# Kernel tuning notes

Hardware: AMD Instinct MI355X
Metric: run time of the kernel (lower is better)

Reference implementation:

```python
import jax, jax.numpy as jnp
from jax import lax
import numpy as np

B, C, L, K = 8, 512, 2048, 3
CQ = C // 8


def setup_inputs() -> dict:
    key = jax.random.key(0)
    k1, k2, k3, k4 = jax.random.split(key, 4)
    scale = 0.05
    return {
        "x": jax.random.normal(k1, (B, C, L), dtype=jnp.float32),
        "Wq": jax.random.normal(k2, (CQ, C, K), dtype=jnp.float32) * scale,
        "Wk": jax.random.normal(k3, (CQ, C, K), dtype=jnp.float32) * scale,
        "Wv": jax.random.normal(k4, (C, C, K), dtype=jnp.float32) * scale,
        "gamma": jnp.ones((1,), dtype=jnp.float32),
    }


def _conv1d(x, w):
    # x: [B, Cin, L], w: [Cout, Cin, K]; 'same' padding = (K-1)//2 on both sides
    pad = (w.shape[-1] - 1) // 2
    return lax.conv_general_dilated(
        x, w, window_strides=(1,), padding=[(pad, pad)],
        dimension_numbers=("NCH", "OIH", "NCH"))


def reference(x, Wq, Wk, Wv, gamma):
    q = _conv1d(x, Wq)  # [B, C/8, L]
    k = _conv1d(x, Wk)  # [B, C/8, L]
    v = _conv1d(x, Wv)  # [B, C, L]
    # scores[b, i, j] = sum_c q[b, c, i] * k[b, c, j]  (q^T k)
    scores = jnp.einsum("bci,bcj->bij", q, k)
    # softmax over dim=1 (the query/i axis) — non-standard axis
    beta = jax.nn.softmax(scores, axis=1)  # [B, L, L]
    out = gamma * jnp.einsum("bcl,blj->bcj", v, beta)  # [B, C, L]
    return out
```

## Files before the change

kernel.cpp:

```cpp
#include <hip/hip_runtime.h>
#include <cstddef>
#include <math.h>

#define L_DIM 2048
#define C_DIM 512
#define CQ_DIM 64
#define B_DIM 8

typedef _Float16 f16x8 __attribute__((ext_vector_type(8)));
typedef __fp16 fp16x2_t __attribute__((ext_vector_type(2)));
typedef float f32x4 __attribute__((ext_vector_type(4)));

__device__ __forceinline__ unsigned short f2h(float f) {
    union { _Float16 h; unsigned short u; } v;
    v.h = (_Float16)f;
    return v.u;
}

__device__ __forceinline__ unsigned p2u(float a, float b) {
    union { fp16x2_t h; unsigned u; } v;
    v.h = __builtin_amdgcn_cvt_pkrtz(a, b);
    return v.u;
}

__global__ __launch_bounds__(256) void prep_w(const float* __restrict__ Wq,
                                              const float* __restrict__ Wk,
                                              const float* __restrict__ Wv,
                                              unsigned short* __restrict__ Wh) {
    const int idx = blockIdx.x * 256 + threadIdx.x;
    const int ci = idx & 511;
    const int co = (idx >> 9) % 640;
    const int t  = idx / (640 * 512);
    float w;
    if (co < 64)       w = Wq[(size_t)co * 1536 + ci * 3 + t];
    else if (co < 128) w = Wk[(size_t)(co - 64) * 1536 + ci * 3 + t];
    else               w = Wv[(size_t)(co - 128) * 1536 + ci * 3 + t];
    Wh[idx] = f2h(w);
}

__global__ __launch_bounds__(256) void prep_x(const float* __restrict__ x,
                                              unsigned short* __restrict__ xT) {
    const int l0  = blockIdx.x * 64;
    const int ci0 = blockIdx.y * 64;
    const int b   = blockIdx.z;

    __shared__ float xs[64][68];
    const int tid = threadIdx.x;
    const float* xb = x + ((size_t)b * C_DIM + ci0) * L_DIM;

    for (int idx = tid; idx < 64 * 16; idx += 256) {
        int ci = idx >> 4, lq = idx & 15;
        *(float4*)&xs[ci][lq * 4] = *(const float4*)&xb[(size_t)ci * L_DIM + l0 + lq * 4];
    }
    __syncthreads();

    unsigned short* ob = xT + ((size_t)b * L_DIM + l0) * C_DIM + ci0;
    for (int idx = tid; idx < 64 * 8; idx += 256) {
        int l = idx >> 3, c8 = idx & 7;
        ushort4 r0, r1;
        r0.x = f2h(xs[c8 * 8 + 0][l]); r0.y = f2h(xs[c8 * 8 + 1][l]);
        r0.z = f2h(xs[c8 * 8 + 2][l]); r0.w = f2h(xs[c8 * 8 + 3][l]);
        r1.x = f2h(xs[c8 * 8 + 4][l]); r1.y = f2h(xs[c8 * 8 + 5][l]);
        r1.z = f2h(xs[c8 * 8 + 6][l]); r1.w = f2h(xs[c8 * 8 + 7][l]);
        *(ushort4*)&ob[(size_t)l * C_DIM + c8 * 8] = r0;
        *(ushort4*)&ob[(size_t)l * C_DIM + c8 * 8 + 4] = r1;
    }
}

__global__ __launch_bounds__(256) void conv_all(const unsigned short* __restrict__ Wh,
                                                const unsigned short* __restrict__ xT,
                                                unsigned short* __restrict__ qT,
                                                unsigned short* __restrict__ kT,
                                                unsigned short* __restrict__ vB) {
    const int l0  = blockIdx.x * 128;
    const int co0 = blockIdx.y * 64;
    const int b   = blockIdx.z;

    __shared__ unsigned short As[3][64][40];
    __shared__ unsigned short Bs[130][40];

    const int tid  = threadIdx.x;
    const int lane = tid & 63, w = tid >> 6;
    const int ln15 = lane & 15, quad = lane >> 4;

    const int co_w = (w & 1) * 32;
    const int l_w  = (w >> 1) * 64;

    const unsigned short* xb = xT + (size_t)b * L_DIM * C_DIM;

    f32x4 acc[2][4] = {};

    for (int ci0 = 0; ci0 < C_DIM; ci0 += 32) {
        __syncthreads();
        for (int idx = tid; idx < 768; idx += 256) {
            int t = idx >> 8, co = (idx >> 2) & 63, c8 = idx & 3;
            *(float4*)&As[t][co][c8 * 8] =
                *(const float4*)&Wh[(((size_t)t * 640) + co0 + co) * C_DIM + ci0 + c8 * 8];
        }
        for (int idx = tid; idx < 520; idx += 256) {
            int la = idx >> 2, c8 = idx & 3;
            int l = l0 - 1 + la;
            float4 vx = {0.f, 0.f, 0.f, 0.f};
            if (l >= 0 && l < L_DIM)
                vx = *(const float4*)&xb[(size_t)l * C_DIM + ci0 + c8 * 8];
            *(float4*)&Bs[la][c8 * 8] = vx;
        }
        __syncthreads();

#pragma unroll
        for (int t = 0; t < 3; t++) {
            f16x8 a[2], bfr[4];
#pragma unroll
            for (int ct = 0; ct < 2; ct++)
                a[ct] = *(const f16x8*)&As[t][co_w + ct * 16 + ln15][quad * 8];
#pragma unroll
            for (int lt = 0; lt < 4; lt++)
                bfr[lt] = *(const f16x8*)&Bs[l_w + lt * 16 + ln15 + t][quad * 8];
#pragma unroll
            for (int ct = 0; ct < 2; ct++)
#pragma unroll
                for (int lt = 0; lt < 4; lt++)
                    acc[ct][lt] = __builtin_amdgcn_mfma_f32_16x16x32_f16(a[ct], bfr[lt], acc[ct][lt], 0, 0, 0);
        }
    }

    if (co0 < 128) {
        unsigned short* dst = (co0 == 0 ? qT : kT) + (size_t)b * L_DIM * CQ_DIM;
#pragma unroll
        for (int ct = 0; ct < 2; ct++)
#pragma unroll
            for (int lt = 0; lt < 4; lt++) {
                const int l = l0 + l_w + lt * 16 + ln15;
                ushort4 r;
                r.x = f2h(acc[ct][lt][0]); r.y = f2h(acc[ct][lt][1]);
                r.z = f2h(acc[ct][lt][2]); r.w = f2h(acc[ct][lt][3]);
                *(ushort4*)&dst[(size_t)l * CQ_DIM + co_w + ct * 16 + quad * 4] = r;
            }
    } else {
        unsigned short* dst = vB + ((size_t)b * C_DIM + (co0 - 128)) * L_DIM;
#pragma unroll
        for (int ct = 0; ct < 2; ct++)
#pragma unroll
            for (int lt = 0; lt < 4; lt++) {
                const int l = l0 + l_w + lt * 16 + ln15;
#pragma unroll
                for (int r = 0; r < 4; r++) {
                    const int co = co_w + ct * 16 + quad * 4 + r;
                    dst[(size_t)co * L_DIM + l] = f2h(acc[ct][lt][r]);
                }
            }
    }
}

__global__ __launch_bounds__(256) void stat_k(const unsigned short* __restrict__ qT,
                                              const unsigned short* __restrict__ kT,
                                              float* __restrict__ pstat) {
    const int ich = blockIdx.x;
    const int j0  = blockIdx.y * 64;
    const int b   = blockIdx.z;

    __shared__ unsigned short sbuf[64 * 68];

    const int tid = threadIdx.x;
    const int lane = tid & 63, w = tid >> 6;
    const int ln15 = lane & 15, quad = lane >> 4;
    const int sj = w * 16;

    const unsigned short* qb = qT + (size_t)b * L_DIM * CQ_DIM;
    const unsigned short* kb = kT + (size_t)b * L_DIM * CQ_DIM;

    for (int idx = tid; idx < 64 * 8; idx += 256) {
        int r = idx >> 3, c8 = idx & 7;
        *(float4*)&sbuf[r * 68 + c8 * 8] = *(const float4*)&kb[(size_t)(j0 + r) * CQ_DIM + c8 * 8];
    }
    __syncthreads();
    f16x8 kfr[2];
#pragma unroll
    for (int cc = 0; cc < 2; cc++)
        kfr[cc] = *(const f16x8*)&sbuf[(sj + ln15) * 68 + cc * 32 + quad * 8];

    float m_run = -1e30f, l_run = 0.f;

    for (int t = 0; t < 4; t++) {
        const int i0 = ich * 256 + t * 64;
        __syncthreads();
        for (int idx = tid; idx < 64 * 8; idx += 256) {
            int r = idx >> 3, c8 = idx & 7;
            *(float4*)&sbuf[r * 68 + c8 * 8] = *(const float4*)&qb[(size_t)(i0 + r) * CQ_DIM + c8 * 8];
        }
        __syncthreads();

        f32x4 sacc[4] = {};
#pragma unroll
        for (int cc = 0; cc < 2; cc++) {
#pragma unroll
            for (int it = 0; it < 4; it++) {
                const f16x8 afr = *(const f16x8*)&sbuf[(it * 16 + ln15) * 68 + cc * 32 + quad * 8];
                sacc[it] = __builtin_amdgcn_mfma_f32_16x16x32_f16(afr, kfr[cc], sacc[it], 0, 0, 0);
            }
        }

        float bm = -1e30f;
#pragma unroll
        for (int it = 0; it < 4; it++)
#pragma unroll
            for (int r = 0; r < 4; r++)
                bm = fmaxf(bm, sacc[it][r]);
        bm = fmaxf(bm, __shfl_xor(bm, 16, 64));
        bm = fmaxf(bm, __shfl_xor(bm, 32, 64));
        const float m_new = fmaxf(m_run, bm);
        const float alpha = __expf(m_run - m_new);

        float lsum = 0.f;
#pragma unroll
        for (int it = 0; it < 4; it++) {
            float p0 = __expf(sacc[it][0] - m_new);
            float p1 = __expf(sacc[it][1] - m_new);
            float p2 = __expf(sacc[it][2] - m_new);
            float p3 = __expf(sacc[it][3] - m_new);
            lsum += (p0 + p1) + (p2 + p3);
        }
        lsum += __shfl_xor(lsum, 16, 64);
        lsum += __shfl_xor(lsum, 32, 64);
        l_run = l_run * alpha + lsum;
        m_run = m_new;
    }

    if (quad == 0) {
        const int j = j0 + sj + ln15;
        float* pm = pstat;
        float* pl = pstat + 8 * 8 * 2048;
        pm[((size_t)ich * 8 + b) * 2048 + j] = m_run;
        pl[((size_t)ich * 8 + b) * 2048 + j] = l_run;
    }
}

__global__ __launch_bounds__(256) void pv2(const unsigned short* __restrict__ qT,
                                           const unsigned short* __restrict__ kT,
                                           const unsigned short* __restrict__ vB,
                                           const float* __restrict__ pstat,
                                           const float* __restrict__ gamma,
                                           float* __restrict__ out) {
    const int j0  = blockIdx.x * 64;
    const int co0 = blockIdx.y * 128;
    const int b   = blockIdx.z;

    __shared__ unsigned short pps[64 * 68];
    __shared__ unsigned short qTs[64 * 68];
    __shared__ unsigned short vvs[128 * 68];
    __shared__ float mj_s[64];
    __shared__ float il_s[64];

    const int tid = threadIdx.x;
    const int lane = tid & 63, w = tid >> 6;
    const int ln15 = lane & 15, quad = lane >> 4;

    const unsigned short* qb = qT + (size_t)b * L_DIM * CQ_DIM;
    const unsigned short* kb = kT + (size_t)b * L_DIM * CQ_DIM;
    const unsigned short* vb = vB + (size_t)b * C_DIM * L_DIM;

    const int sj  = w * 16;
    const int wco = w * 32;

    if (tid < 64) {
        const int j = j0 + tid;
        const float* pm = pstat;
        const float* pl = pstat + 8 * 8 * 2048;
        float m = -1e30f;
        float pmv[8];
#pragma unroll
        for (int c = 0; c < 8; c++) {
            pmv[c] = pm[((size_t)c * 8 + b) * 2048 + j];
            m = fmaxf(m, pmv[c]);
        }
        float l = 0.f;
#pragma unroll
        for (int c = 0; c < 8; c++)
            l = fmaf(pl[((size_t)c * 8 + b) * 2048 + j], __expf(pmv[c] - m), l);
        mj_s[tid] = m;
        il_s[tid] = gamma[0] / l;
    }

    for (int idx = tid; idx < 64 * 8; idx += 256) {
        int r = idx >> 3, c8 = idx & 7;
        *(float4*)&pps[r * 68 + c8 * 8] = *(const float4*)&kb[(size_t)(j0 + r) * CQ_DIM + c8 * 8];
    }
    __syncthreads();
    f16x8 kfr[2];
#pragma unroll
    for (int cc = 0; cc < 2; cc++)
        kfr[cc] = *(const f16x8*)&pps[(sj + ln15) * 68 + cc * 32 + quad * 8];
    const float m_lane = mj_s[sj + ln15];
    float inv[4];
#pragma unroll
    for (int bb = 0; bb < 4; bb++)
        inv[bb] = il_s[bb * 16 + ln15];

    f32x4 oacc[2][4] = {};

    for (int i0 = 0; i0 < L_DIM; i0 += 64) {
        __syncthreads();
        for (int idx = tid; idx < 64 * 8; idx += 256) {
            int r = idx >> 3, c8 = idx & 7;
            *(float4*)&qTs[r * 68 + c8 * 8] = *(const float4*)&qb[(size_t)(i0 + r) * CQ_DIM + c8 * 8];
        }
        for (int idx = tid; idx < 128 * 8; idx += 256) {
            int r = idx >> 3, c8 = idx & 7;
            *(float4*)&vvs[r * 68 + c8 * 8] = *(const float4*)&vb[(size_t)(co0 + r) * L_DIM + i0 + c8 * 8];
        }
        __syncthreads();

        f32x4 sacc[4] = {};
        __builtin_amdgcn_s_setprio(1);
#pragma unroll
        for (int cc = 0; cc < 2; cc++) {
#pragma unroll
            for (int it = 0; it < 4; it++) {
                const f16x8 afr = *(const f16x8*)&qTs[(it * 16 + ln15) * 68 + cc * 32 + quad * 8];
                sacc[it] = __builtin_amdgcn_mfma_f32_16x16x32_f16(afr, kfr[cc], sacc[it], 0, 0, 0);
            }
        }
        __builtin_amdgcn_s_setprio(0);

        const int j = sj + ln15;
#pragma unroll
        for (int it = 0; it < 4; it++) {
            float p0 = __expf(sacc[it][0] - m_lane);
            float p1 = __expf(sacc[it][1] - m_lane);
            float p2 = __expf(sacc[it][2] - m_lane);
            float p3 = __expf(sacc[it][3] - m_lane);
            uint2 u;
            u.x = p2u(p0, p1);
            u.y = p2u(p2, p3);
            *(uint2*)&pps[j * 68 + it * 16 + quad * 4] = u;
        }
        __syncthreads();

#pragma unroll
        for (int cc = 0; cc < 2; cc++) {
            f16x8 afr[2], bfr[4];
#pragma unroll
            for (int t = 0; t < 2; t++)
                afr[t] = *(const f16x8*)&vvs[(wco + t * 16 + ln15) * 68 + cc * 32 + quad * 8];
#pragma unroll
            for (int t = 0; t < 4; t++)
                bfr[t] = *(const f16x8*)&pps[(t * 16 + ln15) * 68 + cc * 32 + quad * 8];
            __builtin_amdgcn_s_setprio(1);
#pragma unroll
            for (int a = 0; a < 2; a++)
#pragma unroll
                for (int bb = 0; bb < 4; bb++)
                    oacc[a][bb] = __builtin_amdgcn_mfma_f32_16x16x32_f16(afr[a], bfr[bb], oacc[a][bb], 0, 0, 0);
            __builtin_amdgcn_s_setprio(0);
        }
    }

#pragma unroll
    for (int a = 0; a < 2; a++)
#pragma unroll
        for (int r = 0; r < 4; r++) {
            const int co = co0 + wco + a * 16 + quad * 4 + r;
            float* ob = out + ((size_t)b * C_DIM + co) * L_DIM + j0;
#pragma unroll
            for (int bb = 0; bb < 4; bb++)
                ob[bb * 16 + ln15] = oacc[a][bb][r] * inv[bb];
        }
}

extern "C" void kernel_launch(void* const* d_in, const int* in_sizes, int n_in,
                              void* d_out, int out_size, void* d_ws, size_t ws_size,
                              hipStream_t stream) {
    const float* x     = (const float*)d_in[0];
    const float* Wq    = (const float*)d_in[1];
    const float* Wk    = (const float*)d_in[2];
    const float* Wv    = (const float*)d_in[3];
    const float* gamma = (const float*)d_in[4];
    float* out = (float*)d_out;

    unsigned short* ws_h = (unsigned short*)d_ws;
    unsigned short* qT = ws_h;
    unsigned short* kT = qT + 1048576;
    unsigned short* vB = kT + 1048576;
    unsigned short* xT = vB + 8388608;
    unsigned short* Wh = xT + 8388608;
    float* pstat = (float*)xT;

    prep_w  <<<3840, 256, 0, stream>>>(Wq, Wk, Wv, Wh);
    prep_x  <<<dim3(32, 8, 8), 256, 0, stream>>>(x, xT);
    conv_all<<<dim3(16, 10, 8), 256, 0, stream>>>(Wh, xT, qT, kT, vB);
    stat_k  <<<dim3(8, 32, 8), 256, 0, stream>>>(qT, kT, pstat);
    pv2     <<<dim3(32, 4, 8), 256, 0, stream>>>(qT, kT, vB, pstat, gamma, out);
}
```

Baseline: 269.9 us.

## Prefetch next Q/V tiles into registers and make each wave own its P columns

Each wave now computes the PV product for all 128 output channels on its own 16 columns of P. Because a wave only reads the P rows it wrote, the barrier between the softmax write and the PV MMAs can be dropped. The next iteration's Q and V tiles are also loaded into registers while the current tile is computed, which overlaps global latency with the MMAs. In exchange, each wave re-reads the full V tile from LDS every iteration and register pressure rises from the prefetch buffers and eight accumulators, which could reduce occupancy.

```diff
diff --git a/kernel.cpp b/kernel.cpp
--- a/kernel.cpp
+++ b/kernel.cpp
@@ -259,8 +259,7 @@
     const unsigned short* kb = kT + (size_t)b * L_DIM * CQ_DIM;
     const unsigned short* vb = vB + (size_t)b * C_DIM * L_DIM;
 
-    const int sj  = w * 16;
-    const int wco = w * 32;
+    const int sj = w * 16;
 
     if (tid < 64) {
         const int j = j0 + tid;
@@ -290,25 +289,37 @@
 #pragma unroll
     for (int cc = 0; cc < 2; cc++)
         kfr[cc] = *(const f16x8*)&pps[(sj + ln15) * 68 + cc * 32 + quad * 8];
-    const float m_lane = mj_s[sj + ln15];
-    float inv[4];
-#pragma unroll
-    for (int bb = 0; bb < 4; bb++)
-        inv[bb] = il_s[bb * 16 + ln15];
-
-    f32x4 oacc[2][4] = {};
+    const float m_lane   = mj_s[sj + ln15];
+    const float inv_lane = il_s[sj + ln15];
+
+    f32x4 oacc[8] = {};
+
+    const int sr = tid >> 3;
+    const int sc = (tid & 7) * 8;
+    float4 rq[2], rv[4];
+    rq[0] = *(const float4*)&qb[(size_t)sr * CQ_DIM + sc];
+    rq[1] = *(const float4*)&qb[(size_t)(sr + 32) * CQ_DIM + sc];
+#pragma unroll
+    for (int k = 0; k < 4; k++)
+        rv[k] = *(const float4*)&vb[(size_t)(co0 + sr + 32 * k) * L_DIM + sc];
 
     for (int i0 = 0; i0 < L_DIM; i0 += 64) {
         __syncthreads();
-        for (int idx = tid; idx < 64 * 8; idx += 256) {
-            int r = idx >> 3, c8 = idx & 7;
-            *(float4*)&qTs[r * 68 + c8 * 8] = *(const float4*)&qb[(size_t)(i0 + r) * CQ_DIM + c8 * 8];
-        }
-        for (int idx = tid; idx < 128 * 8; idx += 256) {
-            int r = idx >> 3, c8 = idx & 7;
-            *(float4*)&vvs[r * 68 + c8 * 8] = *(const float4*)&vb[(size_t)(co0 + r) * L_DIM + i0 + c8 * 8];
-        }
-        __syncthreads();
+        *(float4*)&qTs[sr * 68 + sc] = rq[0];
+        *(float4*)&qTs[(sr + 32) * 68 + sc] = rq[1];
+#pragma unroll
+        for (int k = 0; k < 4; k++)
+            *(float4*)&vvs[(sr + 32 * k) * 68 + sc] = rv[k];
+        __syncthreads();
+
+        if (i0 + 64 < L_DIM) {
+            const int i1 = i0 + 64;
+            rq[0] = *(const float4*)&qb[(size_t)(i1 + sr) * CQ_DIM + sc];
+            rq[1] = *(const float4*)&qb[(size_t)(i1 + sr + 32) * CQ_DIM + sc];
+#pragma unroll
+            for (int k = 0; k < 4; k++)
+                rv[k] = *(const float4*)&vb[(size_t)(co0 + sr + 32 * k) * L_DIM + i1 + sc];
+        }
 
         f32x4 sacc[4] = {};
         __builtin_amdgcn_s_setprio(1);
@@ -334,36 +345,26 @@
             u.y = p2u(p2, p3);
             *(uint2*)&pps[j * 68 + it * 16 + quad * 4] = u;
         }
-        __syncthreads();
-
-#pragma unroll
-        for (int cc = 0; cc < 2; cc++) {
-            f16x8 afr[2], bfr[4];
-#pragma unroll
-            for (int t = 0; t < 2; t++)
-                afr[t] = *(const f16x8*)&vvs[(wco + t * 16 + ln15) * 68 + cc * 32 + quad * 8];
-#pragma unroll
-            for (int t = 0; t < 4; t++)
-                bfr[t] = *(const f16x8*)&pps[(t * 16 + ln15) * 68 + cc * 32 + quad * 8];
-            __builtin_amdgcn_s_setprio(1);
-#pragma unroll
-            for (int a = 0; a < 2; a++)
-#pragma unroll
-                for (int bb = 0; bb < 4; bb++)
-                    oacc[a][bb] = __builtin_amdgcn_mfma_f32_16x16x32_f16(afr[a], bfr[bb], oacc[a][bb], 0, 0, 0);
-            __builtin_amdgcn_s_setprio(0);
-        }
-    }
-
-#pragma unroll
-    for (int a = 0; a < 2; a++)
+
+        __builtin_amdgcn_s_setprio(1);
+#pragma unroll
+        for (int ks = 0; ks < 2; ks++) {
+            const f16x8 bfr = *(const f16x8*)&pps[(sj + ln15) * 68 + ks * 32 + quad * 8];
+#pragma unroll
+            for (int a = 0; a < 8; a++) {
+                const f16x8 afr = *(const f16x8*)&vvs[(a * 16 + ln15) * 68 + ks * 32 + quad * 8];
+                oacc[a] = __builtin_amdgcn_mfma_f32_16x16x32_f16(afr, bfr, oacc[a], 0, 0, 0);
+            }
+        }
+        __builtin_amdgcn_s_setprio(0);
+    }
+
+#pragma unroll
+    for (int a = 0; a < 8; a++)
 #pragma unroll
         for (int r = 0; r < 4; r++) {
-            const int co = co0 + wco + a * 16 + quad * 4 + r;
-            float* ob = out + ((size_t)b * C_DIM + co) * L_DIM + j0;
-#pragma unroll
-            for (int bb = 0; bb < 4; bb++)
-                ob[bb * 16 + ln15] = oacc[a][bb][r] * inv[bb];
+            const int co = co0 + a * 16 + quad * 4 + r;
+            out[((size_t)b * C_DIM + co) * L_DIM + j0 + sj + ln15] = oacc[a][r] * inv_lane;
         }
 }
 
```

Measured after the change: 384.9 us. 42.6% more time.

## Load Q and V fragments directly from global, fold log2e into Q

Applied to the files above, without the earlier changes.

Q and V tiles are no longer staged through shared memory in the stats and PV kernels. MFMA operand fragments are read straight from global memory (L2/cache), which removes two barriers and the LDS copy per iteration. Q is pre-scaled by log2(e) at projection time so the softmax can use exp2f instead of __expf. The trade-off is more redundant global loads across waves and uncoalesced 16-byte reads, with no staging to hide latency. The exp computation is also moved before the barrier that guards the shared P tile.

```diff
diff --git a/kernel.cpp b/kernel.cpp
--- a/kernel.cpp
+++ b/kernel.cpp
@@ -6,6 +6,7 @@
 #define C_DIM 512
 #define CQ_DIM 64
 #define B_DIM 8
+#define LOG2E 1.44269504088896340736f
 
 typedef _Float16 f16x8 __attribute__((ext_vector_type(8)));
 typedef __fp16 fp16x2_t __attribute__((ext_vector_type(2)));
@@ -125,6 +126,7 @@
     }
 
     if (co0 < 128) {
+        const float qs = (co0 == 0) ? LOG2E : 1.0f;
         unsigned short* dst = (co0 == 0 ? qT : kT) + (size_t)b * L_DIM * CQ_DIM;
 #pragma unroll
         for (int ct = 0; ct < 2; ct++)
@@ -132,8 +134,8 @@
             for (int lt = 0; lt < 4; lt++) {
                 const int l = l0 + l_w + lt * 16 + ln15;
                 ushort4 r;
-                r.x = f2h(acc[ct][lt][0]); r.y = f2h(acc[ct][lt][1]);
-                r.z = f2h(acc[ct][lt][2]); r.w = f2h(acc[ct][lt][3]);
+                r.x = f2h(acc[ct][lt][0] * qs); r.y = f2h(acc[ct][lt][1] * qs);
+                r.z = f2h(acc[ct][lt][2] * qs); r.w = f2h(acc[ct][lt][3] * qs);
                 *(ushort4*)&dst[(size_t)l * CQ_DIM + co_w + ct * 16 + quad * 4] = r;
             }
     } else {
@@ -183,19 +185,13 @@
 
     for (int t = 0; t < 4; t++) {
         const int i0 = ich * 256 + t * 64;
-        __syncthreads();
-        for (int idx = tid; idx < 64 * 8; idx += 256) {
-            int r = idx >> 3, c8 = idx & 7;
-            *(float4*)&sbuf[r * 68 + c8 * 8] = *(const float4*)&qb[(size_t)(i0 + r) * CQ_DIM + c8 * 8];
-        }
-        __syncthreads();
 
         f32x4 sacc[4] = {};
 #pragma unroll
         for (int cc = 0; cc < 2; cc++) {
 #pragma unroll
             for (int it = 0; it < 4; it++) {
-                const f16x8 afr = *(const f16x8*)&sbuf[(it * 16 + ln15) * 68 + cc * 32 + quad * 8];
+                const f16x8 afr = *(const f16x8*)&qb[(size_t)(i0 + it * 16 + ln15) * CQ_DIM + cc * 32 + quad * 8];
                 sacc[it] = __builtin_amdgcn_mfma_f32_16x16x32_f16(afr, kfr[cc], sacc[it], 0, 0, 0);
             }
         }
@@ -209,15 +205,15 @@
         bm = fmaxf(bm, __shfl_xor(bm, 16, 64));
         bm = fmaxf(bm, __shfl_xor(bm, 32, 64));
         const float m_new = fmaxf(m_run, bm);
-        const float alpha = __expf(m_run - m_new);
+        const float alpha = exp2f(m_run - m_new);
 
         float lsum = 0.f;
 #pragma unroll
         for (int it = 0; it < 4; it++) {
-            float p0 = __expf(sacc[it][0] - m_new);
-            float p1 = __expf(sacc[it][1] - m_new);
-            float p2 = __expf(sacc[it][2] - m_new);
-            float p3 = __expf(sacc[it][3] - m_new);
+            float p0 = exp2f(sacc[it][0] - m_new);
+            float p1 = exp2f(sacc[it][1] - m_new);
+            float p2 = exp2f(sacc[it][2] - m_new);
+            float p3 = exp2f(sacc[it][3] - m_new);
             lsum += (p0 + p1) + (p2 + p3);
         }
         lsum += __shfl_xor(lsum, 16, 64);
@@ -246,8 +242,6 @@
     const int b   = blockIdx.z;
 
     __shared__ unsigned short pps[64 * 68];
-    __shared__ unsigned short qTs[64 * 68];
-    __shared__ unsigned short vvs[128 * 68];
     __shared__ float mj_s[64];
     __shared__ float il_s[64];
 
@@ -276,7 +270,7 @@
         float l = 0.f;
 #pragma unroll
         for (int c = 0; c < 8; c++)
-            l = fmaf(pl[((size_t)c * 8 + b) * 2048 + j], __expf(pmv[c] - m), l);
+            l = fmaf(pl[((size_t)c * 8 + b) * 2048 + j], exp2f(pmv[c] - m), l);
         mj_s[tid] = m;
         il_s[tid] = gamma[0] / l;
     }
@@ -299,60 +293,53 @@
     f32x4 oacc[2][4] = {};
 
     for (int i0 = 0; i0 < L_DIM; i0 += 64) {
-        __syncthreads();
-        for (int idx = tid; idx < 64 * 8; idx += 256) {
-            int r = idx >> 3, c8 = idx & 7;
-            *(float4*)&qTs[r * 68 + c8 * 8] = *(const float4*)&qb[(size_t)(i0 + r) * CQ_DIM + c8 * 8];
-        }
-        for (int idx = tid; idx < 128 * 8; idx += 256) {
-            int r = idx >> 3, c8 = idx & 7;
-            *(float4*)&vvs[r * 68 + c8 * 8] = *(const float4*)&vb[(size_t)(co0 + r) * L_DIM + i0 + c8 * 8];
-        }
-        __syncthreads();
-
         f32x4 sacc[4] = {};
         __builtin_amdgcn_s_setprio(1);
 #pragma unroll
         for (int cc = 0; cc < 2; cc++) {
 #pragma unroll
             for (int it = 0; it < 4; it++) {
-                const f16x8 afr = *(const f16x8*)&qTs[(it * 16 + ln15) * 68 + cc * 32 + quad * 8];
+                const f16x8 afr = *(const f16x8*)&qb[(size_t)(i0 + it * 16 + ln15) * CQ_DIM + cc * 32 + quad * 8];
                 sacc[it] = __builtin_amdgcn_mfma_f32_16x16x32_f16(afr, kfr[cc], sacc[it], 0, 0, 0);
             }
         }
         __builtin_amdgcn_s_setprio(0);
 
+        uint2 pu[4];
+#pragma unroll
+        for (int it = 0; it < 4; it++) {
+            float p0 = exp2f(sacc[it][0] - m_lane);
+            float p1 = exp2f(sacc[it][1] - m_lane);
+            float p2 = exp2f(sacc[it][2] - m_lane);
+            float p3 = exp2f(sacc[it][3] - m_lane);
+            pu[it].x = p2u(p0, p1);
+            pu[it].y = p2u(p2, p3);
+        }
+
+        __syncthreads();
         const int j = sj + ln15;
 #pragma unroll
-        for (int it = 0; it < 4; it++) {
-            float p0 = __expf(sacc[it][0] - m_lane);
-            float p1 = __expf(sacc[it][1] - m_lane);
-            float p2 = __expf(sacc[it][2] - m_lane);
-            float p3 = __expf(sacc[it][3] - m_lane);
-            uint2 u;
-            u.x = p2u(p0, p1);
-            u.y = p2u(p2, p3);
-            *(uint2*)&pps[j * 68 + it * 16 + quad * 4] = u;
-        }
+        for (int it = 0; it < 4; it++)
+            *(uint2*)&pps[j * 68 + it * 16 + quad * 4] = pu[it];
         __syncthreads();
 
+        __builtin_amdgcn_s_setprio(1);
 #pragma unroll
         for (int cc = 0; cc < 2; cc++) {
             f16x8 afr[2], bfr[4];
 #pragma unroll
             for (int t = 0; t < 2; t++)
-                afr[t] = *(const f16x8*)&vvs[(wco + t * 16 + ln15) * 68 + cc * 32 + quad * 8];
+                afr[t] = *(const f16x8*)&vb[(size_t)(co0 + wco + t * 16 + ln15) * L_DIM + i0 + cc * 32 + quad * 8];
 #pragma unroll
             for (int t = 0; t < 4; t++)
                 bfr[t] = *(const f16x8*)&pps[(t * 16 + ln15) * 68 + cc * 32 + quad * 8];
-            __builtin_amdgcn_s_setprio(1);
 #pragma unroll
             for (int a = 0; a < 2; a++)
 #pragma unroll
                 for (int bb = 0; bb < 4; bb++)
                     oacc[a][bb] = __builtin_amdgcn_mfma_f32_16x16x32_f16(afr[a], bfr[bb], oacc[a][bb], 0, 0, 0);
-            __builtin_amdgcn_s_setprio(0);
-        }
+        }
+        __builtin_amdgcn_s_setprio(0);
     }
 
 #pragma unroll
```

New measurement: 363.5 us. +34.7%, slower.
